# Optimization experiments

Hardware: AMD Instinct MI355X
Metric: run time of the kernel (lower is better)

Reference implementation:

```python
import jax, jax.numpy as jnp
import numpy as np

B, S, ENC2, DEC = 32, 4096, 1024, 512

def setup_inputs() -> dict:
    key = jax.random.key(0)
    k1, k2, k3 = jax.random.split(key, 3)
    hidden = jax.random.normal(k1, (B, DEC), dtype=jnp.float32)
    context = jax.random.normal(k2, (B, S, ENC2), dtype=jnp.float32)
    mask = jnp.ones((B, S), dtype=jnp.int32)
    # Linear(enc*2+dec -> dec): weight [DEC, ENC2+DEC], bias [DEC]
    W_attn = jax.random.normal(k3, (DEC, ENC2 + DEC), dtype=jnp.float32) * (1.0 / np.sqrt(ENC2 + DEC))
    b_attn = jnp.zeros((DEC,), dtype=jnp.float32)
    v = jax.random.uniform(jax.random.fold_in(key, 7), (DEC,), dtype=jnp.float32)
    return {"hidden": hidden, "context": context, "mask": mask,
            "W_attn": W_attn, "b_attn": b_attn, "v": v}

def reference(hidden, context, mask, W_attn, b_attn, v):
    # cat((hidden repeated over S, context)) @ W.T == hidden@Wh.T + context@Wc.T
    # split W to avoid materializing the [B,S,1536] concat
    Wh = W_attn[:, :DEC]          # acts on hidden (first in cat)
    Wc = W_attn[:, DEC:]          # acts on context
    h_proj = hidden @ Wh.T + b_attn                      # [B, DEC]
    c_proj = jnp.einsum('bse,de->bsd', context, Wc)      # [B, S, DEC]
    sim = jnp.tanh(h_proj[:, None, :] + c_proj)          # [B, S, DEC]
    scores = jnp.einsum('bsd,d->bs', sim, v)             # [B, S]
    scores = jnp.where(mask == 0, -jnp.inf, scores)
    return jax.nn.softmax(scores, axis=1)
```

## Files before the change

### kernel.cpp

```cpp
#include <hip/hip_runtime.h>
#include <hip/hip_bf16.h>
#include <cmath>

#define NB 32
#define NS 4096
#define NK 1024
#define ND 512
#define WSTRIDE 1536
#define NT 32

using bf16x8 = __attribute__((ext_vector_type(8))) __bf16;
using u16x8  = __attribute__((ext_vector_type(8))) unsigned short;
using f32x4  = __attribute__((ext_vector_type(4))) float;
typedef unsigned short u16;

__device__ inline u16 f2b(float x) {
    __hip_bfloat16 h = __float2bfloat16(x);
    u16 u; __builtin_memcpy(&u, &h, 2); return u;
}

__device__ inline float fast_tanh(float x) {
    float xc = fminf(fmaxf(x, -10.f), 10.f);
    float e = __expf(2.f * xc);
    return (e - 1.f) / (e + 1.f);
}

__global__ void pack_wc_kernel(const float* __restrict__ W, u16* __restrict__ wcb) {
    int idx = blockIdx.x * 256 + threadIdx.x;
    int R = idx >> 10, k = idx & 1023;
    float val = W[(size_t)R * WSTRIDE + ND + k];
    int ks = k >> 5, S = (k >> 3) & 3, j = k & 7;
    int g = ((R << 2) + S) ^ (R & 7);
    wcb[(ks << 14) + (g << 3) + j] = f2b(val);
}

__global__ void hproj_kernel(const float* __restrict__ hidden, const float* __restrict__ W,
                             const float* __restrict__ bias, float* __restrict__ hp) {
    int b = blockIdx.x, d = threadIdx.x;
    __shared__ float sh[ND];
    sh[d] = hidden[b * ND + d];
    __syncthreads();
    const float4* wr = (const float4*)(W + (size_t)d * WSTRIDE);
    float acc = bias[d];
#pragma unroll 8
    for (int k = 0; k < ND / 4; k++) {
        float4 w4 = wr[k];
        acc += w4.x * sh[4 * k] + w4.y * sh[4 * k + 1] + w4.z * sh[4 * k + 2] + w4.w * sh[4 * k + 3];
    }
    hp[b * ND + d] = acc;
}

__global__ __launch_bounds__(512, 2)
void fused_scores_kernel(const float* __restrict__ ctx, const u16* __restrict__ wcb,
                         const float* __restrict__ hp, const float* __restrict__ vvec,
                         float* __restrict__ scores) {
    __shared__ __align__(16) char lA[2][128 * 64];
    __shared__ __align__(16) char lB[2][512 * 64];
    __shared__ float shHp[ND];
    __shared__ float shV[ND];
    __shared__ float shSc[4][128];

    const int tid = threadIdx.x;
    const int blk = blockIdx.x;
    const int b  = blk >> 5;
    const int s0 = (blk & 31) << 7;

    shHp[tid] = hp[b * ND + tid];
    shV[tid]  = vvec[tid];

    const int lane = tid & 63, wid = tid >> 6;
    const int l15 = lane & 15, l4 = lane >> 4;
    const int wm = wid >> 2, wn = wid & 3;

    const int srow = tid >> 2, q = tid & 3;
    const float4* asrc = (const float4*)(ctx + (size_t)b * NS * NK + (size_t)(s0 + srow) * NK);
    const int awbyte = ((srow << 6) + (q << 4)) ^ ((srow & 7) << 4);

    int aoff[4], boff[8];
#pragma unroll
    for (int r = 0; r < 4; r++) {
        int row = (wm << 6) + (r << 4) + l15;
        aoff[r] = ((row << 6) + (l4 << 4)) ^ ((row & 7) << 4);
    }
#pragma unroll
    for (int c = 0; c < 8; c++) {
        int row = (wn << 7) + (c << 4) + l15;
        boff[c] = ((row << 6) + (l4 << 4)) ^ ((row & 7) << 4);
    }

    f32x4 acc[4][8];
    f32x4 zero = {0.f, 0.f, 0.f, 0.f};
#pragma unroll
    for (int r = 0; r < 4; r++)
#pragma unroll
        for (int c = 0; c < 8; c++) acc[r][c] = zero;

    const char* wcb_bytes = (const char*)wcb;
    float4 va0, va1;

#pragma unroll
    for (int i = 0; i < 4; i++) {
        const char* src = wcb_bytes + ((((((wid << 2) + i) << 6) + lane)) << 4);
        __builtin_amdgcn_global_load_lds(
            (const __attribute__((address_space(1))) void*)src,
            (__attribute__((address_space(3))) void*)(&lB[0][((wid << 2) + i) << 10]),
            16, 0, 0);
    }
    va0 = asrc[q << 1];
    va1 = asrc[(q << 1) + 1];
    asm volatile("s_waitcnt vmcnt(0)" ::: "memory");
    {
        u16x8 a8;
        a8[0] = f2b(va0.x); a8[1] = f2b(va0.y); a8[2] = f2b(va0.z); a8[3] = f2b(va0.w);
        a8[4] = f2b(va1.x); a8[5] = f2b(va1.y); a8[6] = f2b(va1.z); a8[7] = f2b(va1.w);
        *(u16x8*)(&lA[0][awbyte]) = a8;
    }
    va0 = asrc[8 + (q << 1)];
    va1 = asrc[8 + (q << 1) + 1];
    asm volatile("s_waitcnt lgkmcnt(0)" ::: "memory");
    __builtin_amdgcn_s_barrier();
    __builtin_amdgcn_sched_barrier(0);

#pragma unroll 2
    for (int t = 0; t < NT; t++) {
        const int cur = t & 1, nxt = cur ^ 1;
        const int tB = (t + 1 < NT) ? t + 1 : NT - 1;
        const int tA = (t + 2 < NT) ? t + 2 : NT - 1;

#pragma unroll
        for (int i = 0; i < 4; i++) {
            const char* src = wcb_bytes + ((size_t)tB << 15)
                              + (((((wid << 2) + i) << 6) + lane) << 4);
            __builtin_amdgcn_global_load_lds(
                (const __attribute__((address_space(1))) void*)src,
                (__attribute__((address_space(3))) void*)(&lB[nxt][((wid << 2) + i) << 10]),
                16, 0, 0);
        }
        asm volatile("s_waitcnt vmcnt(4)" ::: "memory");
        {
            u16x8 a8;
            a8[0] = f2b(va0.x); a8[1] = f2b(va0.y); a8[2] = f2b(va0.z); a8[3] = f2b(va0.w);
            a8[4] = f2b(va1.x); a8[5] = f2b(va1.y); a8[6] = f2b(va1.z); a8[7] = f2b(va1.w);
            *(u16x8*)(&lA[nxt][awbyte]) = a8;
        }
        va0 = asrc[(tA << 3) + (q << 1)];
        va1 = asrc[(tA << 3) + (q << 1) + 1];

        bf16x8 af[4], bfr[8];
#pragma unroll
        for (int r = 0; r < 4; r++) af[r] = *(const bf16x8*)(&lA[cur][aoff[r]]);
#pragma unroll
        for (int c = 0; c < 8; c++) bfr[c] = *(const bf16x8*)(&lB[cur][boff[c]]);
#pragma unroll
        for (int r = 0; r < 4; r++)
#pragma unroll
            for (int c = 0; c < 8; c++)
                acc[r][c] = __builtin_amdgcn_mfma_f32_16x16x32_bf16(af[r], bfr[c], acc[r][c], 0, 0, 0);

        asm volatile("s_waitcnt vmcnt(2) lgkmcnt(0)" ::: "memory");
        __builtin_amdgcn_s_barrier();
        __builtin_amdgcn_sched_barrier(0);
    }

    float part[4][4];
#pragma unroll
    for (int r = 0; r < 4; r++)
#pragma unroll
        for (int i = 0; i < 4; i++) part[r][i] = 0.f;

#pragma unroll
    for (int r = 0; r < 4; r++) {
#pragma unroll
        for (int c = 0; c < 8; c++) {
            int d = (wn << 7) + (c << 4) + l15;
            float hpv = shHp[d], vv = shV[d];
#pragma unroll
            for (int i = 0; i < 4; i++) {
                float x = acc[r][c][i] + hpv;
                part[r][i] += fast_tanh(x) * vv;
            }
        }
    }

#pragma unroll
    for (int r = 0; r < 4; r++) {
#pragma unroll
        for (int i = 0; i < 4; i++) {
            float p = part[r][i];
            p += __shfl_xor(p, 1); p += __shfl_xor(p, 2);
            p += __shfl_xor(p, 4); p += __shfl_xor(p, 8);
            if (l15 == 0) shSc[wn][(wm << 6) + (r << 4) + (l4 << 2) + i] = p;
        }
    }
    __syncthreads();
    if (tid < 128) {
        float s = shSc[0][tid] + shSc[1][tid] + shSc[2][tid] + shSc[3][tid];
        scores[(size_t)b * NS + s0 + tid] = s;
    }
}

__global__ void softmax_kernel(const float* __restrict__ scores, const int* __restrict__ mask,
                               float* __restrict__ out) {
    int b = blockIdx.x, tid = threadIdx.x;
    __shared__ float red[256];
    float loc[16];
    float mx = -INFINITY;
#pragma unroll
    for (int i = 0; i < 16; i++) {
        int idx = i * 256 + tid;
        float s = scores[b * NS + idx];
        if (mask[b * NS + idx] == 0) s = -INFINITY;
        loc[i] = s;
        mx = fmaxf(mx, s);
    }
    red[tid] = mx; __syncthreads();
    for (int off = 128; off; off >>= 1) { if (tid < off) red[tid] = fmaxf(red[tid], red[tid + off]); __syncthreads(); }
    mx = red[0]; __syncthreads();
    float sum = 0.f;
#pragma unroll
    for (int i = 0; i < 16; i++) { float e = __expf(loc[i] - mx); loc[i] = e; sum += e; }
    red[tid] = sum; __syncthreads();
    for (int off = 128; off; off >>= 1) { if (tid < off) red[tid] += red[tid + off]; __syncthreads(); }
    float inv = 1.f / red[0];
#pragma unroll
    for (int i = 0; i < 16; i++) out[b * NS + i * 256 + tid] = loc[i] * inv;
}

extern "C" void kernel_launch(void* const* d_in, const int* in_sizes, int n_in,
                              void* d_out, int out_size, void* d_ws, size_t ws_size,
                              hipStream_t stream) {
    const float* hidden  = (const float*)d_in[0];
    const float* context = (const float*)d_in[1];
    const int*   mask    = (const int*)d_in[2];
    const float* W_attn  = (const float*)d_in[3];
    const float* b_attn  = (const float*)d_in[4];
    const float* v       = (const float*)d_in[5];
    float* out           = (float*)d_out;

    char* ws = (char*)d_ws;
    u16*   wcb    = (u16*)ws;
    float* hp     = (float*)(ws + (1 << 20));
    float* scores = (float*)(ws + (1 << 20) + (64 << 10));

    pack_wc_kernel<<<2048, 256, 0, stream>>>(W_attn, wcb);
    hproj_kernel<<<NB, ND, 0, stream>>>(hidden, W_attn, b_attn, hp);
    fused_scores_kernel<<<NB * 32, 512, 0, stream>>>(context, wcb, hp, v, scores);
    softmax_kernel<<<NB, 256, 0, stream>>>(scores, mask, out);
}
```

Measured before the change: 299.9 us.

## Split MFMA loop into four barrier-synced phases with priority-boosted compute clusters

The main GEMM loop is restructured into four phases, each loading two B fragments from LDS and running eight MFMAs bracketed by s_setprio and workgroup barriers. The A-tile convert/write and global prefetch are moved into the second phase so memory traffic is interleaved with compute. This is a ping-pong-style schedule meant to keep the matrix units fed and overlap loads with MFMAs. It adds many extra barriers per iteration, which could cost more than it gains with only 8 waves and 2 blocks per CU.

New measurement: 314.5 us. 4.9% more time.

```diff
diff --git a/kernel.cpp b/kernel.cpp
--- a/kernel.cpp
+++ b/kernel.cpp
@@ -98,23 +98,30 @@
     const char* wcb_bytes = (const char*)wcb;
     float4 va0, va1;
 
-#pragma unroll
-    for (int i = 0; i < 4; i++) {
-        const char* src = wcb_bytes + ((((((wid << 2) + i) << 6) + lane)) << 4);
-        __builtin_amdgcn_global_load_lds(
-            (const __attribute__((address_space(1))) void*)src,
-            (__attribute__((address_space(3))) void*)(&lB[0][((wid << 2) + i) << 10]),
-            16, 0, 0);
-    }
+#define STAGE_B_DMA(tile, buf)                                                       \
+    _Pragma("unroll")                                                                \
+    for (int i = 0; i < 4; i++) {                                                    \
+        const char* src = wcb_bytes + ((size_t)(tile) << 15)                         \
+                          + (((((wid << 2) + i) << 6) + lane) << 4);                 \
+        __builtin_amdgcn_global_load_lds(                                            \
+            (const __attribute__((address_space(1))) void*)src,                      \
+            (__attribute__((address_space(3))) void*)(&lB[buf][((wid << 2) + i) << 10]), \
+            16, 0, 0);                                                               \
+    }
+
+#define CVT_WRITE_A(buf)                                                             \
+    {                                                                                \
+        u16x8 a8;                                                                    \
+        a8[0] = f2b(va0.x); a8[1] = f2b(va0.y); a8[2] = f2b(va0.z); a8[3] = f2b(va0.w); \
+        a8[4] = f2b(va1.x); a8[5] = f2b(va1.y); a8[6] = f2b(va1.z); a8[7] = f2b(va1.w); \
+        *(u16x8*)(&lA[buf][awbyte]) = a8;                                            \
+    }
+
+    STAGE_B_DMA(0, 0);
     va0 = asrc[q << 1];
     va1 = asrc[(q << 1) + 1];
     asm volatile("s_waitcnt vmcnt(0)" ::: "memory");
-    {
-        u16x8 a8;
-        a8[0] = f2b(va0.x); a8[1] = f2b(va0.y); a8[2] = f2b(va0.z); a8[3] = f2b(va0.w);
-        a8[4] = f2b(va1.x); a8[5] = f2b(va1.y); a8[6] = f2b(va1.z); a8[7] = f2b(va1.w);
-        *(u16x8*)(&lA[0][awbyte]) = a8;
-    }
+    CVT_WRITE_A(0);
     va0 = asrc[8 + (q << 1)];
     va1 = asrc[8 + (q << 1) + 1];
     asm volatile("s_waitcnt lgkmcnt(0)" ::: "memory");
@@ -127,39 +134,84 @@
         const int tB = (t + 1 < NT) ? t + 1 : NT - 1;
         const int tA = (t + 2 < NT) ? t + 2 : NT - 1;
 
-#pragma unroll
-        for (int i = 0; i < 4; i++) {
-            const char* src = wcb_bytes + ((size_t)tB << 15)
-                              + (((((wid << 2) + i) << 6) + lane) << 4);
-            __builtin_amdgcn_global_load_lds(
-                (const __attribute__((address_space(1))) void*)src,
-                (__attribute__((address_space(3))) void*)(&lB[nxt][((wid << 2) + i) << 10]),
-                16, 0, 0);
-        }
-        asm volatile("s_waitcnt vmcnt(4)" ::: "memory");
+        bf16x8 af[4];
+
+        STAGE_B_DMA(tB, nxt);
+#pragma unroll
+        for (int r = 0; r < 4; r++) af[r] = *(const bf16x8*)(&lA[cur][aoff[r]]);
         {
-            u16x8 a8;
-            a8[0] = f2b(va0.x); a8[1] = f2b(va0.y); a8[2] = f2b(va0.z); a8[3] = f2b(va0.w);
-            a8[4] = f2b(va1.x); a8[5] = f2b(va1.y); a8[6] = f2b(va1.z); a8[7] = f2b(va1.w);
-            *(u16x8*)(&lA[nxt][awbyte]) = a8;
-        }
-        va0 = asrc[(tA << 3) + (q << 1)];
-        va1 = asrc[(tA << 3) + (q << 1) + 1];
-
-        bf16x8 af[4], bfr[8];
-#pragma unroll
-        for (int r = 0; r < 4; r++) af[r] = *(const bf16x8*)(&lA[cur][aoff[r]]);
-#pragma unroll
-        for (int c = 0; c < 8; c++) bfr[c] = *(const bf16x8*)(&lB[cur][boff[c]]);
-#pragma unroll
-        for (int r = 0; r < 4; r++)
-#pragma unroll
-            for (int c = 0; c < 8; c++)
-                acc[r][c] = __builtin_amdgcn_mfma_f32_16x16x32_bf16(af[r], bfr[c], acc[r][c], 0, 0, 0);
-
-        asm volatile("s_waitcnt vmcnt(2) lgkmcnt(0)" ::: "memory");
-        __builtin_amdgcn_s_barrier();
-        __builtin_amdgcn_sched_barrier(0);
+            bf16x8 b0 = *(const bf16x8*)(&lB[cur][boff[0]]);
+            bf16x8 b1 = *(const bf16x8*)(&lB[cur][boff[1]]);
+            asm volatile("s_waitcnt vmcnt(6)" ::: "memory");
+            __builtin_amdgcn_s_barrier();
+            asm volatile("s_waitcnt lgkmcnt(0)" ::: "memory");
+            __builtin_amdgcn_sched_barrier(0);
+            __builtin_amdgcn_s_setprio(1);
+#pragma unroll
+            for (int r = 0; r < 4; r++)
+                acc[r][0] = __builtin_amdgcn_mfma_f32_16x16x32_bf16(af[r], b0, acc[r][0], 0, 0, 0);
+#pragma unroll
+            for (int r = 0; r < 4; r++)
+                acc[r][1] = __builtin_amdgcn_mfma_f32_16x16x32_bf16(af[r], b1, acc[r][1], 0, 0, 0);
+            __builtin_amdgcn_s_setprio(0);
+            __builtin_amdgcn_s_barrier();
+        }
+
+        {
+            bf16x8 b2 = *(const bf16x8*)(&lB[cur][boff[2]]);
+            bf16x8 b3 = *(const bf16x8*)(&lB[cur][boff[3]]);
+            asm volatile("s_waitcnt vmcnt(4)" ::: "memory");
+            CVT_WRITE_A(nxt);
+            va0 = asrc[(tA << 3) + (q << 1)];
+            va1 = asrc[(tA << 3) + (q << 1) + 1];
+            __builtin_amdgcn_s_barrier();
+            asm volatile("s_waitcnt lgkmcnt(0)" ::: "memory");
+            __builtin_amdgcn_sched_barrier(0);
+            __builtin_amdgcn_s_setprio(1);
+#pragma unroll
+            for (int r = 0; r < 4; r++)
+                acc[r][2] = __builtin_amdgcn_mfma_f32_16x16x32_bf16(af[r], b2, acc[r][2], 0, 0, 0);
+#pragma unroll
+            for (int r = 0; r < 4; r++)
+                acc[r][3] = __builtin_amdgcn_mfma_f32_16x16x32_bf16(af[r], b3, acc[r][3], 0, 0, 0);
+            __builtin_amdgcn_s_setprio(0);
+            __builtin_amdgcn_s_barrier();
+        }
+
+        {
+            bf16x8 b4 = *(const bf16x8*)(&lB[cur][boff[4]]);
+            bf16x8 b5 = *(const bf16x8*)(&lB[cur][boff[5]]);
+            __builtin_amdgcn_s_barrier();
+            asm volatile("s_waitcnt lgkmcnt(0)" ::: "memory");
+            __builtin_amdgcn_sched_barrier(0);
+            __builtin_amdgcn_s_setprio(1);
+#pragma unroll
+            for (int r = 0; r < 4; r++)
+                acc[r][4] = __builtin_amdgcn_mfma_f32_16x16x32_bf16(af[r], b4, acc[r][4], 0, 0, 0);
+#pragma unroll
+            for (int r = 0; r < 4; r++)
+                acc[r][5] = __builtin_amdgcn_mfma_f32_16x16x32_bf16(af[r], b5, acc[r][5], 0, 0, 0);
+            __builtin_amdgcn_s_setprio(0);
+            __builtin_amdgcn_s_barrier();
+        }
+
+        {
+            bf16x8 b6 = *(const bf16x8*)(&lB[cur][boff[6]]);
+            bf16x8 b7 = *(const bf16x8*)(&lB[cur][boff[7]]);
+            asm volatile("s_waitcnt vmcnt(4)" ::: "memory");
+            __builtin_amdgcn_s_barrier();
+            asm volatile("s_waitcnt lgkmcnt(0)" ::: "memory");
+            __builtin_amdgcn_sched_barrier(0);
+            __builtin_amdgcn_s_setprio(1);
+#pragma unroll
+            for (int r = 0; r < 4; r++)
+                acc[r][6] = __builtin_amdgcn_mfma_f32_16x16x32_bf16(af[r], b6, acc[r][6], 0, 0, 0);
+#pragma unroll
+            for (int r = 0; r < 4; r++)
+                acc[r][7] = __builtin_amdgcn_mfma_f32_16x16x32_bf16(af[r], b7, acc[r][7], 0, 0, 0);
+            __builtin_amdgcn_s_setprio(0);
+            __builtin_amdgcn_s_barrier();
+        }
     }
 
     float part[4][4];
```

## Widen A tile to 64 K per stage and split into two MFMA sub-steps

Applied to the files above, without the earlier changes.

The context (A) tile is widened to 64 K-elements per LDS buffer, so the fp32-to-bf16 convert, store and A refill happen once every two 32-wide MFMA sub-steps, while B still double-buffers at 32-K granularity. MFMA clusters are wrapped in s_setprio to favour the compute wave, and launch bounds drop to one block per CU to fit the larger LDS footprint. The aim is fewer A pipeline stages and wider A loads per thread. The cost is halved occupancy and a more delicate vmcnt accounting across the two sub-steps.

Result: no change. 298.5 us (-0.5%).

```diff
diff --git a/kernel.cpp b/kernel.cpp
--- a/kernel.cpp
+++ b/kernel.cpp
@@ -7,7 +7,7 @@
 #define NK 1024
 #define ND 512
 #define WSTRIDE 1536
-#define NT 32
+#define NTO 16
 
 using bf16x8 = __attribute__((ext_vector_type(8))) __bf16;
 using u16x8  = __attribute__((ext_vector_type(8))) unsigned short;
@@ -50,11 +50,11 @@
     hp[b * ND + d] = acc;
 }
 
-__global__ __launch_bounds__(512, 2)
+__global__ __launch_bounds__(512, 1)
 void fused_scores_kernel(const float* __restrict__ ctx, const u16* __restrict__ wcb,
                          const float* __restrict__ hp, const float* __restrict__ vvec,
                          float* __restrict__ scores) {
-    __shared__ __align__(16) char lA[2][128 * 64];
+    __shared__ __align__(16) char lA[2][128 * 128];
     __shared__ __align__(16) char lB[2][512 * 64];
     __shared__ float shHp[ND];
     __shared__ float shV[ND];
@@ -74,13 +74,14 @@
 
     const int srow = tid >> 2, q = tid & 3;
     const float4* asrc = (const float4*)(ctx + (size_t)b * NS * NK + (size_t)(s0 + srow) * NK);
-    const int awbyte = ((srow << 6) + (q << 4)) ^ ((srow & 7) << 4);
+    const int awb0 = (srow << 7) + ((((q << 1) + 0) ^ (srow & 7)) << 4);
+    const int awb1 = (srow << 7) + ((((q << 1) + 1) ^ (srow & 7)) << 4);
 
     int aoff[4], boff[8];
 #pragma unroll
     for (int r = 0; r < 4; r++) {
         int row = (wm << 6) + (r << 4) + l15;
-        aoff[r] = ((row << 6) + (l4 << 4)) ^ ((row & 7) << 4);
+        aoff[r] = (row << 7) + ((l4 ^ (row & 7)) << 4);
     }
 #pragma unroll
     for (int c = 0; c < 8; c++) {
@@ -96,70 +97,84 @@
         for (int c = 0; c < 8; c++) acc[r][c] = zero;
 
     const char* wcb_bytes = (const char*)wcb;
-    float4 va0, va1;
-
-#pragma unroll
-    for (int i = 0; i < 4; i++) {
-        const char* src = wcb_bytes + ((((((wid << 2) + i) << 6) + lane)) << 4);
-        __builtin_amdgcn_global_load_lds(
-            (const __attribute__((address_space(1))) void*)src,
-            (__attribute__((address_space(3))) void*)(&lB[0][((wid << 2) + i) << 10]),
-            16, 0, 0);
-    }
-    va0 = asrc[q << 1];
-    va1 = asrc[(q << 1) + 1];
+    float4 va[4];
+
+#define STAGE_B_DMA(chunk, buf)                                                      \
+    _Pragma("unroll")                                                                \
+    for (int i = 0; i < 4; i++) {                                                    \
+        const char* src = wcb_bytes + ((size_t)(chunk) << 15)                        \
+                          + (((((wid << 2) + i) << 6) + lane) << 4);                 \
+        __builtin_amdgcn_global_load_lds(                                            \
+            (const __attribute__((address_space(1))) void*)src,                      \
+            (__attribute__((address_space(3))) void*)(&lB[buf][((wid << 2) + i) << 10]), \
+            16, 0, 0);                                                               \
+    }
+
+#define LOAD_A_REGS(tile)                                                            \
+    _Pragma("unroll")                                                                \
+    for (int i = 0; i < 4; i++) va[i] = asrc[((tile) << 4) + (q << 2) + i];
+
+#define CVT_WRITE_A(buf)                                                             \
+    {                                                                                \
+        u16x8 lo, hi;                                                                \
+        lo[0] = f2b(va[0].x); lo[1] = f2b(va[0].y); lo[2] = f2b(va[0].z); lo[3] = f2b(va[0].w); \
+        lo[4] = f2b(va[1].x); lo[5] = f2b(va[1].y); lo[6] = f2b(va[1].z); lo[7] = f2b(va[1].w); \
+        hi[0] = f2b(va[2].x); hi[1] = f2b(va[2].y); hi[2] = f2b(va[2].z); hi[3] = f2b(va[2].w); \
+        hi[4] = f2b(va[3].x); hi[5] = f2b(va[3].y); hi[6] = f2b(va[3].z); hi[7] = f2b(va[3].w); \
+        *(u16x8*)(&lA[buf][awb0]) = lo;                                              \
+        *(u16x8*)(&lA[buf][awb1]) = hi;                                              \
+    }
+
+#define MFMA_CLUSTER(abuf, axor, bbuf)                                               \
+    {                                                                                \
+        bf16x8 af[4], bfr[8];                                                        \
+        _Pragma("unroll")                                                            \
+        for (int r = 0; r < 4; r++) af[r] = *(const bf16x8*)(&lA[abuf][aoff[r] ^ (axor)]); \
+        _Pragma("unroll")                                                            \
+        for (int c = 0; c < 8; c++) bfr[c] = *(const bf16x8*)(&lB[bbuf][boff[c]]);   \
+        __builtin_amdgcn_s_setprio(1);                                               \
+        _Pragma("unroll")                                                            \
+        for (int r = 0; r < 4; r++)                                                  \
+            _Pragma("unroll")                                                        \
+            for (int c = 0; c < 8; c++)                                              \
+                acc[r][c] = __builtin_amdgcn_mfma_f32_16x16x32_bf16(af[r], bfr[c], acc[r][c], 0, 0, 0); \
+        __builtin_amdgcn_s_setprio(0);                                               \
+    }
+
+    STAGE_B_DMA(0, 0);
+    LOAD_A_REGS(0);
     asm volatile("s_waitcnt vmcnt(0)" ::: "memory");
-    {
-        u16x8 a8;
-        a8[0] = f2b(va0.x); a8[1] = f2b(va0.y); a8[2] = f2b(va0.z); a8[3] = f2b(va0.w);
-        a8[4] = f2b(va1.x); a8[5] = f2b(va1.y); a8[6] = f2b(va1.z); a8[7] = f2b(va1.w);
-        *(u16x8*)(&lA[0][awbyte]) = a8;
-    }
-    va0 = asrc[8 + (q << 1)];
-    va1 = asrc[8 + (q << 1) + 1];
+    CVT_WRITE_A(0);
+    LOAD_A_REGS(1);
     asm volatile("s_waitcnt lgkmcnt(0)" ::: "memory");
     __builtin_amdgcn_s_barrier();
     __builtin_amdgcn_sched_barrier(0);
 
 #pragma unroll 2
-    for (int t = 0; t < NT; t++) {
-        const int cur = t & 1, nxt = cur ^ 1;
-        const int tB = (t + 1 < NT) ? t + 1 : NT - 1;
-        const int tA = (t + 2 < NT) ? t + 2 : NT - 1;
-
-#pragma unroll
-        for (int i = 0; i < 4; i++) {
-            const char* src = wcb_bytes + ((size_t)tB << 15)
-                              + (((((wid << 2) + i) << 6) + lane) << 4);
-            __builtin_amdgcn_global_load_lds(
-                (const __attribute__((address_space(1))) void*)src,
-                (__attribute__((address_space(3))) void*)(&lB[nxt][((wid << 2) + i) << 10]),
-                16, 0, 0);
-        }
-        asm volatile("s_waitcnt vmcnt(4)" ::: "memory");
+    for (int t = 0; t < NTO; t++) {
+        const int curA = t & 1, nxtA = curA ^ 1;
+        const int u0 = t << 1;
+
         {
-            u16x8 a8;
-            a8[0] = f2b(va0.x); a8[1] = f2b(va0.y); a8[2] = f2b(va0.z); a8[3] = f2b(va0.w);
-            a8[4] = f2b(va1.x); a8[5] = f2b(va1.y); a8[6] = f2b(va1.z); a8[7] = f2b(va1.w);
-            *(u16x8*)(&lA[nxt][awbyte]) = a8;
-        }
-        va0 = asrc[(tA << 3) + (q << 1)];
-        va1 = asrc[(tA << 3) + (q << 1) + 1];
-
-        bf16x8 af[4], bfr[8];
-#pragma unroll
-        for (int r = 0; r < 4; r++) af[r] = *(const bf16x8*)(&lA[cur][aoff[r]]);
-#pragma unroll
-        for (int c = 0; c < 8; c++) bfr[c] = *(const bf16x8*)(&lB[cur][boff[c]]);
-#pragma unroll
-        for (int r = 0; r < 4; r++)
-#pragma unroll
-            for (int c = 0; c < 8; c++)
-                acc[r][c] = __builtin_amdgcn_mfma_f32_16x16x32_bf16(af[r], bfr[c], acc[r][c], 0, 0, 0);
-
-        asm volatile("s_waitcnt vmcnt(2) lgkmcnt(0)" ::: "memory");
-        __builtin_amdgcn_s_barrier();
-        __builtin_amdgcn_sched_barrier(0);
+            const int cB = (u0 + 1 < 32) ? u0 + 1 : 31;
+            STAGE_B_DMA(cB, 1);
+            asm volatile("s_waitcnt vmcnt(4)" ::: "memory");
+            CVT_WRITE_A(nxtA);
+            const int tA = (t + 2 < NTO) ? t + 2 : NTO - 1;
+            LOAD_A_REGS(tA);
+            MFMA_CLUSTER(curA, 0, 0);
+            asm volatile("s_waitcnt vmcnt(4) lgkmcnt(0)" ::: "memory");
+            __builtin_amdgcn_s_barrier();
+            __builtin_amdgcn_sched_barrier(0);
+        }
+        {
+            const int cB = (u0 + 2 < 32) ? u0 + 2 : 31;
+            STAGE_B_DMA(cB, 0);
+            MFMA_CLUSTER(curA, 64, 1);
+            asm volatile("s_waitcnt vmcnt(4) lgkmcnt(0)" ::: "memory");
+            __builtin_amdgcn_s_barrier();
+            __builtin_amdgcn_sched_barrier(0);
+        }
     }
 
     float part[4][4];
```
